# Optimization experiments

Measured on AMD Instinct MI355X. Metric: run time of the kernel, lower is better.

## Reference

```python
import jax, jax.numpy as jnp
import numpy as np

N_HEADS = 16

def setup_inputs() -> dict:
    key = jax.random.key(0)
    ks = jax.random.split(key, 6)
    B, L, D = 1, 2048, 1024
    M = 2048  # max_len
    dh = D // N_HEADS
    s = 0.02
    return {
        "x": jax.random.normal(ks[0], (B, L, D), jnp.float32),
        "Wqkv": jax.random.normal(ks[1], (D, 3 * D), jnp.float32) * s,
        "bqkv": jax.random.normal(ks[2], (3 * D,), jnp.float32) * s,
        "Wout": jax.random.normal(ks[3], (D, D), jnp.float32) * s,
        "bout": jax.random.normal(ks[4], (D,), jnp.float32) * s,
        "rel_emb": jax.random.normal(ks[5], (2 * M - 1, dh), jnp.float32),
    }

def reference(x, Wqkv, bqkv, Wout, bout, rel_emb):
    B, L, D = x.shape
    H = N_HEADS
    dh = D // H
    qkv = x @ Wqkv + bqkv                       # [B,L,3D]
    q, k, v = jnp.split(qkv, 3, axis=-1)
    q = q.reshape(B, L, H, dh).transpose(0, 2, 1, 3)  # [B,H,L,dh]
    k = k.reshape(B, L, H, dh).transpose(0, 2, 1, 3)
    v = v.reshape(B, L, H, dh).transpose(0, 2, 1, 3)
    content = jnp.einsum('bhid,bhjd->bhij', q, k)      # [B,H,L,L]
    rel = jnp.einsum('bhid,rd->bhir', q, rel_emb)      # [B,H,L,2M-1]
    # _skew: F.pad(x,(1,0)); view keeps shape; slice [...,:L]
    rel = jnp.pad(rel, ((0, 0), (0, 0), (0, 0), (1, 0)))[..., :L]
    scores = (content + rel) / jnp.sqrt(jnp.asarray(dh, x.dtype))
    attn = jax.nn.softmax(scores, axis=-1)
    out = jnp.einsum('bhij,bhjd->bhid', attn, v)       # [B,H,L,dh]
    out = out.transpose(0, 2, 1, 3).reshape(B, L, D)
    return out @ Wout + bout
```

## Files before the change

kernel.cpp:

```cpp
#include <hip/hip_runtime.h>
#include <hip/hip_bf16.h>
#include <stdint.h>

typedef __attribute__((ext_vector_type(8))) __bf16 bf16x8;
typedef __attribute__((ext_vector_type(4))) float f32x4;
typedef __attribute__((ext_vector_type(16))) float f32x16;
typedef __attribute__((ext_vector_type(2))) uint32_t u32x2;

#define MFMA16(a, b, c) __builtin_amdgcn_mfma_f32_16x16x32_bf16(a, b, c, 0, 0, 0)
#define MFMA32(a, b, c) __builtin_amdgcn_mfma_f32_32x32x16_bf16(a, b, c, 0, 0, 0)

typedef const __attribute__((address_space(1))) uint32_t* gas_ptr;
typedef __attribute__((address_space(3))) uint32_t* lds_ptr;

static __device__ __forceinline__ ushort f2b(float f) {
  union { float f; uint32_t u; } x; x.f = f;
  uint32_t u = x.u + 0x7fffu + ((x.u >> 16) & 1u);
  return (ushort)(u >> 16);
}

static __device__ __forceinline__ void g2lds16(const void* g, void* l) {
  __builtin_amdgcn_global_load_lds((gas_ptr)(uintptr_t)g, (lds_ptr)(uintptr_t)l, 16, 0, 0);
}

static __device__ __forceinline__ u32x2 plswap(uint32_t a, uint32_t b) {
  return __builtin_amdgcn_permlane32_swap(a, b, false, false);
}
static __device__ __forceinline__ float xhalf_max(float x) {
  u32x2 r = plswap(__float_as_uint(x), __float_as_uint(x));
  return fmaxf(__uint_as_float(r.x), __uint_as_float(r.y));
}
static __device__ __forceinline__ float xhalf_sum(float x) {
  u32x2 r = plswap(__float_as_uint(x), __float_as_uint(x));
  return __uint_as_float(r.x) + __uint_as_float(r.y);
}

__global__ __launch_bounds__(256) void prep(const float* __restrict__ x, ushort* __restrict__ xb,
                                            const float* __restrict__ Wqkv, ushort* __restrict__ w1t,
                                            const float* __restrict__ Wout, ushort* __restrict__ w2t,
                                            int L) {
  const int b = blockIdx.x, t = threadIdx.x;
  const int ncvt = (L * 1024) / (256 * 4);
  if (b < ncvt) {
    int i = (b * 256 + t) * 4;
    float4 v = *(const float4*)(x + i);
    ushort4 o;
    o.x = f2b(v.x); o.y = f2b(v.y); o.z = f2b(v.z); o.w = f2b(v.w);
    *(ushort4*)(xb + i) = o;
    return;
  }
  __shared__ ushort tile[64][65];
  const float* in; ushort* out; int N; int b2;
  const int K = 1024;
  if (b < ncvt + 768) { b2 = b - ncvt; N = 3072; in = Wqkv; out = w1t; }
  else                { b2 = b - ncvt - 768; N = 1024; in = Wout; out = w2t; }
  int nx = b2 % (N >> 6), ky = b2 / (N >> 6);
  int n0 = nx * 64, k0 = ky * 64;
#pragma unroll
  for (int i = 0; i < 16; ++i) {
    int idx = i * 256 + t;
    int r = idx >> 6, c = idx & 63;
    tile[r][c] = f2b(in[(size_t)(k0 + r) * N + n0 + c]);
  }
  __syncthreads();
#pragma unroll
  for (int i = 0; i < 16; ++i) {
    int idx = i * 256 + t;
    int r = idx >> 6, c = idx & 63;
    out[(size_t)(n0 + r) * K + k0 + c] = tile[c][r];
  }
}

template <int BM, int BN, bool BIAS>
__global__ __launch_bounds__(256) void gemm_dbuf(const ushort* __restrict__ A,
                                                 const ushort* __restrict__ Bt,
                                                 float* __restrict__ C,
                                                 const float* __restrict__ bias,
                                                 int M, int N, int K) {
  constexpr int WM = BM / 2, WN = BN / 2, MF = WM / 16, NF = WN / 16;
  constexpr int AI = BM / 32, BI = BN / 32;
  __shared__ ushort lA[2][BM * 64];
  __shared__ ushort lB[2][BN * 64];
  const int t = threadIdx.x, lane = t & 63;
  const int bm = blockIdx.y * BM, bn = blockIdx.x * BN;
  const int wid = t >> 6, wr = wid >> 1, wc = wid & 1;

  f32x4 acc[MF][NF] = {};

  auto STAGE = [&](int bb, int k0) {
#pragma unroll
    for (int i = 0; i < AI; ++i) {
      int ci = i * 256 + t;
      int r = ci >> 3, cs = ci & 7;
      int cg = (cs ^ (r & 7)) * 8;
      g2lds16(A + (size_t)(bm + r) * K + k0 + cg, (ushort*)lA[bb] + ci * 8);
    }
#pragma unroll
    for (int i = 0; i < BI; ++i) {
      int ci = i * 256 + t;
      int r = ci >> 3, cs = ci & 7;
      int cg = (cs ^ (r & 7)) * 8;
      g2lds16(Bt + (size_t)(bn + r) * K + k0 + cg, (ushort*)lB[bb] + ci * 8);
    }
  };

  STAGE(0, 0);
  asm volatile("s_waitcnt vmcnt(0)" ::: "memory");
  __builtin_amdgcn_s_barrier();
  __builtin_amdgcn_sched_barrier(0);

  const int NS = K >> 6;
  int buf = 0;
  for (int s = 0; s < NS; ++s) {
    if (s + 1 < NS) STAGE(buf ^ 1, (s + 1) << 6);
#pragma unroll
    for (int kk = 0; kk < 2; ++kk) {
      bf16x8 af[MF], bfr[NF];
#pragma unroll
      for (int m = 0; m < MF; ++m) {
        int row = wr * WM + m * 16 + (lane & 15);
        int cb = kk * 64 + ((lane >> 4) << 4);
        int sw = cb ^ ((row & 7) << 4);
        af[m] = *(const bf16x8*)((const char*)lA[buf] + row * 128 + sw);
      }
#pragma unroll
      for (int n = 0; n < NF; ++n) {
        int row = wc * WN + n * 16 + (lane & 15);
        int cb = kk * 64 + ((lane >> 4) << 4);
        int sw = cb ^ ((row & 7) << 4);
        bfr[n] = *(const bf16x8*)((const char*)lB[buf] + row * 128 + sw);
      }
#pragma unroll
      for (int m = 0; m < MF; ++m)
#pragma unroll
        for (int n = 0; n < NF; ++n) acc[m][n] = MFMA16(af[m], bfr[n], acc[m][n]);
    }
    asm volatile("s_waitcnt vmcnt(0)" ::: "memory");
    __builtin_amdgcn_s_barrier();
    __builtin_amdgcn_sched_barrier(0);
    buf ^= 1;
  }
#pragma unroll
  for (int m = 0; m < MF; ++m) {
#pragma unroll
    for (int n = 0; n < NF; ++n) {
      int col = bn + wc * WN + n * 16 + (lane & 15);
      float b = BIAS ? bias[col] : 0.f;
#pragma unroll
      for (int r = 0; r < 4; ++r) {
        int row = bm + wr * WM + m * 16 + ((lane >> 4) << 2) + r;
        C[(size_t)row * N + col] = acc[m][n][r] + b;
      }
    }
  }
}

__global__ __launch_bounds__(256) void gemm_qkv(const ushort* __restrict__ A,
                                                const ushort* __restrict__ Bt,
                                                const float* __restrict__ bqkv,
                                                const float* __restrict__ rel,
                                                ushort* __restrict__ Qs,
                                                ushort* __restrict__ Kp,
                                                ushort* __restrict__ Vt, int M) {
  __shared__ ushort lA[2][128 * 64];
  __shared__ ushort lB[2][128 * 64];
  const int K = 1024;
  const int t = threadIdx.x, lane = t & 63;
  const int bm = blockIdx.y * 128, bn = blockIdx.x * 128;
  const int wid = t >> 6, wr = wid >> 1, wc = wid & 1;

  f32x4 acc[4][4] = {};

  auto STAGE = [&](int bb, int k0) {
#pragma unroll
    for (int i = 0; i < 4; ++i) {
      int ci = i * 256 + t;
      int r = ci >> 3, cs = ci & 7;
      int cg = (cs ^ (r & 7)) * 8;
      g2lds16(A + (size_t)(bm + r) * K + k0 + cg, (ushort*)lA[bb] + ci * 8);
      g2lds16(Bt + (size_t)(bn + r) * K + k0 + cg, (ushort*)lB[bb] + ci * 8);
    }
  };

  STAGE(0, 0);
  asm volatile("s_waitcnt vmcnt(0)" ::: "memory");
  __builtin_amdgcn_s_barrier();
  __builtin_amdgcn_sched_barrier(0);

  int buf = 0;
  for (int s = 0; s < 16; ++s) {
    if (s + 1 < 16) STAGE(buf ^ 1, (s + 1) << 6);
#pragma unroll
    for (int kk = 0; kk < 2; ++kk) {
      bf16x8 af[4], bfr[4];
#pragma unroll
      for (int m = 0; m < 4; ++m) {
        int row = wr * 64 + m * 16 + (lane & 15);
        int cb = kk * 64 + ((lane >> 4) << 4);
        int sw = cb ^ ((row & 7) << 4);
        af[m] = *(const bf16x8*)((const char*)lA[buf] + row * 128 + sw);
      }
#pragma unroll
      for (int n = 0; n < 4; ++n) {
        int row = wc * 64 + n * 16 + (lane & 15);
        int cb = kk * 64 + ((lane >> 4) << 4);
        int sw = cb ^ ((row & 7) << 4);
        bfr[n] = *(const bf16x8*)((const char*)lB[buf] + row * 128 + sw);
      }
#pragma unroll
      for (int m = 0; m < 4; ++m)
#pragma unroll
        for (int n = 0; n < 4; ++n) acc[m][n] = MFMA16(af[m], bfr[n], acc[m][n]);
    }
    asm volatile("s_waitcnt vmcnt(0)" ::: "memory");
    __builtin_amdgcn_s_barrier();
    __builtin_amdgcn_sched_barrier(0);
    buf ^= 1;
  }

  const int sec = bn >> 10;
  const int cis_base = bn & 1023;
  if (sec < 2) {
    ushort* dst = (sec == 0) ? Qs : Kp;
    const float scale = (sec == 0) ? 0.18033688f : 1.0f;
#pragma unroll
    for (int m = 0; m < 4; ++m) {
#pragma unroll
      for (int n = 0; n < 4; ++n) {
        int cis = cis_base + wc * 64 + n * 16 + (lane & 15);
        int hh = cis >> 6, dd = cis & 63;
        float b = bqkv[sec * 1024 + cis];
#pragma unroll
        for (int r = 0; r < 4; ++r) {
          int row = bm + wr * 64 + m * 16 + ((lane >> 4) << 2) + r;
          float v = acc[m][n][r] + b;
          if (sec == 1 && row > 0) v += rel[(size_t)(row - 1) * 64 + dd];
          dst[((size_t)hh * M + row) * 64 + dd] = f2b(v * scale);
        }
      }
    }
  } else {
    char* tb = (char*)lA;
#pragma unroll
    for (int m = 0; m < 4; ++m) {
#pragma unroll
      for (int n = 0; n < 4; ++n) {
        int cl = wc * 64 + n * 16 + (lane & 15);
        int ll = wr * 64 + m * 16 + ((lane >> 4) << 2);
        float b = bqkv[2048 + cis_base + cl];
        ushort4 w4;
        w4.x = f2b(acc[m][n][0] + b);
        w4.y = f2b(acc[m][n][1] + b);
        w4.z = f2b(acc[m][n][2] + b);
        w4.w = f2b(acc[m][n][3] + b);
        *(ushort4*)(tb + cl * 256 + ((ll * 2) ^ ((cl & 15) << 4))) = w4;
      }
    }
    __syncthreads();
#pragma unroll
    for (int ps = 0; ps < 8; ++ps) {
      int cl = ps * 16 + (t >> 4);
      int chunk = t & 15;
      uint4 rv = *(const uint4*)(tb + cl * 256 + ((chunk * 16) ^ ((cl & 15) << 4)));
      *(uint4*)(Vt + (size_t)(cis_base + cl) * M + bm + chunk * 8) = rv;
    }
  }
}

__global__ __launch_bounds__(512) void attn6(const ushort* __restrict__ Qs,
                                             const ushort* __restrict__ Kp,
                                             const ushort* __restrict__ Vt,
                                             ushort* __restrict__ O, int L) {
  __shared__ char smem[69632];
  __shared__ float mls[4][2][32];
  const int bid = blockIdx.x;
  const int h = (bid & 7) * 2 + (bid >> 7);
  const int q0 = ((bid >> 3) & 15) * 128;
  const int t = threadIdx.x, lane = t & 63, w = t >> 6;
  const int qt = w & 3, ks = w >> 2;
  const int ql = lane & 31, hi = lane >> 5;
  const int sw = (ql & 7) << 4;
  const ushort* kh = Kp + (size_t)h * L * 64;
  const ushort* vh = Vt + (size_t)h * 64 * L;
  const int half = L >> 1;
  const int NT = half >> 6;

  bf16x8 qf[4];
  {
    const ushort* qrow = Qs + ((size_t)h * L + q0 + qt * 32 + ql) * 64 + hi * 8;
#pragma unroll
    for (int c = 0; c < 4; ++c) qf[c] = *(const bf16x8*)(qrow + c * 16);
  }

  f32x16 ot0 = {}, ot1 = {};
  float m = -1e30f, l = 0.f;

  auto STAGE = [&](int bb, int tt) {
    char* base = smem + bb * 32768;
#pragma unroll
    for (int s = 0; s < 2; ++s) {
      int kb = s * half + tt * 64;
      char* sb = base + s * 16384;
      {
        int key = t >> 3, pch = t & 7;
        g2lds16(kh + (((size_t)(kb + key)) << 6) + ((pch ^ (key & 7)) << 3), sb + t * 16);
      }
      {
        int d = t >> 3, pch = t & 7;
        g2lds16(vh + (size_t)d * L + kb + ((pch ^ (d & 7)) << 3), sb + 8192 + t * 16);
      }
    }
  };

  STAGE(0, 0);
  asm volatile("s_waitcnt vmcnt(0)" ::: "memory");
  __builtin_amdgcn_s_barrier();
  __builtin_amdgcn_sched_barrier(0);

  int buf = 0;
  for (int tt = 0; tt < NT; ++tt) {
    if (tt + 1 < NT) STAGE(buf ^ 1, tt + 1);
    const char* kbuf = smem + buf * 32768 + ks * 16384;
    const char* vbuf = kbuf + 8192;
    f32x16 s0 = {}, s1 = {};
#pragma unroll
    for (int c = 0; c < 4; ++c) {
      bf16x8 k0 = *(const bf16x8*)(kbuf + ql * 128 + (((2 * c + hi) << 4) ^ sw));
      bf16x8 k1 = *(const bf16x8*)(kbuf + (32 + ql) * 128 + (((2 * c + hi) << 4) ^ sw));
      s0 = MFMA32(k0, qf[c], s0);
      s1 = MFMA32(k1, qf[c], s1);
    }
    float mx = fmaxf(s0[0], s1[0]);
#pragma unroll
    for (int i = 1; i < 16; ++i) mx = fmaxf(fmaxf(s0[i], s1[i]), mx);
    mx = xhalf_max(mx);
    if (!__all(mx - m <= 8.0f)) {
      float mn = fmaxf(m, mx);
      float sc = __builtin_amdgcn_exp2f(m - mn);
      m = mn;
      l *= sc;
      ot0 = ot0 * sc;
      ot1 = ot1 * sc;
    }
    float rs = 0.f;
#pragma unroll
    for (int tl = 0; tl < 2; ++tl) {
      f32x16 s = tl ? s1 : s0;
      float p[16];
      float r0 = 0.f, r1 = 0.f;
#pragma unroll
      for (int i = 0; i < 16; i += 2) {
        p[i] = __builtin_amdgcn_exp2f(s[i] - m);
        p[i + 1] = __builtin_amdgcn_exp2f(s[i + 1] - m);
        r0 += p[i];
        r1 += p[i + 1];
      }
      rs += r0 + r1;
      uint32_t a[8];
#pragma unroll
      for (int i = 0; i < 8; ++i) {
        uint32_t r;
        asm("v_cvt_pk_bf16_f32 %0, %1, %2" : "=v"(r) : "v"(p[2 * i]), "v"(p[2 * i + 1]));
        a[i] = r;
      }
      u32x2 s02 = plswap(a[0], a[2]);
      u32x2 s13 = plswap(a[1], a[3]);
      u32x2 s46 = plswap(a[4], a[6]);
      u32x2 s57 = plswap(a[5], a[7]);
      union { uint32_t u[4]; bf16x8 v; } b0, b1;
      b0.u[0] = s02.x; b0.u[1] = s13.x; b0.u[2] = s02.y; b0.u[3] = s13.y;
      b1.u[0] = s46.x; b1.u[1] = s57.x; b1.u[2] = s46.y; b1.u[3] = s57.y;
      bf16x8 v00 = *(const bf16x8*)(vbuf + ql * 128 + (((tl * 4 + hi) << 4) ^ sw));
      bf16x8 v01 = *(const bf16x8*)(vbuf + ql * 128 + (((tl * 4 + 2 + hi) << 4) ^ sw));
      bf16x8 v10 = *(const bf16x8*)(vbuf + (32 + ql) * 128 + (((tl * 4 + hi) << 4) ^ sw));
      bf16x8 v11 = *(const bf16x8*)(vbuf + (32 + ql) * 128 + (((tl * 4 + 2 + hi) << 4) ^ sw));
      ot0 = MFMA32(v00, b0.v, ot0);
      ot0 = MFMA32(v01, b1.v, ot0);
      ot1 = MFMA32(v10, b0.v, ot1);
      ot1 = MFMA32(v11, b1.v, ot1);
    }
    l += xhalf_sum(rs);
    asm volatile("s_waitcnt vmcnt(0)" ::: "memory");
    __builtin_amdgcn_s_barrier();
    __builtin_amdgcn_sched_barrier(0);
    buf ^= 1;
  }

  float* part = (float*)smem;
  float* merged = (float*)(smem + 4 * 64 * 33 * 4);
  if (ks == 1) {
    if (hi == 0) { mls[qt][0][ql] = m; mls[qt][1][ql] = l; }
    float* pq = part + qt * 64 * 33;
#pragma unroll
    for (int r = 0; r < 16; ++r) {
      int d = (r & 3) + 8 * (r >> 2) + 4 * hi;
      pq[d * 33 + ql] = ot0[r];
      pq[(d + 32) * 33 + ql] = ot1[r];
    }
  }
  __syncthreads();
  if (ks == 0) {
    float m1 = mls[qt][0][ql], l1 = mls[qt][1][ql];
    float mg = fmaxf(m, m1);
    float e0 = __builtin_amdgcn_exp2f(m - mg);
    float e1 = __builtin_amdgcn_exp2f(m1 - mg);
    float inv = 1.0f / (l * e0 + l1 * e1);
    float* pq = part + qt * 64 * 33;
    float* mq = merged + qt * 32 * 68;
#pragma unroll
    for (int r = 0; r < 16; ++r) {
      int d = (r & 3) + 8 * (r >> 2) + 4 * hi;
      mq[ql * 68 + d] = (ot0[r] * e0 + pq[d * 33 + ql] * e1) * inv;
      mq[ql * 68 + 32 + d] = (ot1[r] * e0 + pq[(d + 32) * 33 + ql] * e1) * inv;
    }
  }
  __syncthreads();
#pragma unroll
  for (int pss = 0; pss < 2; ++pss) {
    int id = pss * 512 + t;
    int qt2 = id >> 8, row = (id >> 3) & 31, c8 = id & 7;
    const float* mq = merged + qt2 * 32 * 68 + row * 68 + c8 * 8;
    float4 f0 = *(const float4*)mq;
    float4 f1 = *(const float4*)(mq + 4);
    union { ushort us[8]; uint4 u4; } o;
    o.us[0] = f2b(f0.x); o.us[1] = f2b(f0.y); o.us[2] = f2b(f0.z); o.us[3] = f2b(f0.w);
    o.us[4] = f2b(f1.x); o.us[5] = f2b(f1.y); o.us[6] = f2b(f1.z); o.us[7] = f2b(f1.w);
    *(uint4*)(O + (size_t)(q0 + qt2 * 32 + row) * 1024 + h * 64 + c8 * 8) = o.u4;
  }
}

extern "C" void kernel_launch(void* const* d_in, const int* in_sizes, int n_in,
                              void* d_out, int out_size, void* d_ws, size_t ws_size,
                              hipStream_t stream) {
  (void)n_in; (void)out_size; (void)ws_size;
  const float* x    = (const float*)d_in[0];
  const float* Wqkv = (const float*)d_in[1];
  const float* bqkv = (const float*)d_in[2];
  const float* Wout = (const float*)d_in[3];
  const float* bout = (const float*)d_in[4];
  const float* rel  = (const float*)d_in[5];
  float* out = (float*)d_out;
  const int L = in_sizes[0] / 1024;

  char* ws = (char*)d_ws;
  const size_t MB = 1024 * 1024;
  ushort* xb  = (ushort*)(ws);
  ushort* w1t = (ushort*)(ws + 4 * MB);
  ushort* w2t = (ushort*)(ws + 10 * MB);
  ushort* Qsb = (ushort*)(ws + 36 * MB);
  ushort* Kpb = (ushort*)(ws + 40 * MB);
  ushort* Vtb = (ushort*)(ws + 44 * MB);
  ushort* Ob  = (ushort*)(ws + 48 * MB);

  prep<<<dim3((L * 1024) / 1024 + 768 + 256), 256, 0, stream>>>(x, xb, Wqkv, w1t, Wout, w2t, L);
  gemm_qkv<<<dim3(3072 / 128, L / 128), 256, 0, stream>>>(xb, w1t, bqkv, rel, Qsb, Kpb, Vtb, L);
  attn6<<<dim3((L / 128) * 16), 512, 0, stream>>>(Qsb, Kpb, Vtb, Ob, L);
  gemm_dbuf<128, 64, true><<<dim3(1024 / 64, L / 128), 256, 0, stream>>>(Ob, w2t, out, bout, L, 1024, 1024);
}
```

Baseline: 84.99 us.

## Drop attention key-split, use 256-thread blocks and deferred vmcnt waits in GEMMs

Measured after the change: 87.64 us. 1.03x slower.

```diff
diff --git a/kernel.cpp b/kernel.cpp
--- a/kernel.cpp
+++ b/kernel.cpp
@@ -21,6 +21,13 @@
 
 static __device__ __forceinline__ void g2lds16(const void* g, void* l) {
   __builtin_amdgcn_global_load_lds((gas_ptr)(uintptr_t)g, (lds_ptr)(uintptr_t)l, 16, 0, 0);
+}
+
+template <int N> static __device__ __forceinline__ void waitvm() {
+  if constexpr (N == 0) asm volatile("s_waitcnt vmcnt(0)" ::: "memory");
+  else if constexpr (N == 4) asm volatile("s_waitcnt vmcnt(4)" ::: "memory");
+  else if constexpr (N == 6) asm volatile("s_waitcnt vmcnt(6)" ::: "memory");
+  else if constexpr (N == 8) asm volatile("s_waitcnt vmcnt(8)" ::: "memory");
 }
 
 static __device__ __forceinline__ u32x2 plswap(uint32_t a, uint32_t b) {
@@ -105,14 +112,13 @@
   };
 
   STAGE(0, 0);
-  asm volatile("s_waitcnt vmcnt(0)" ::: "memory");
-  __builtin_amdgcn_s_barrier();
-  __builtin_amdgcn_sched_barrier(0);
-
   const int NS = K >> 6;
   int buf = 0;
   for (int s = 0; s < NS; ++s) {
-    if (s + 1 < NS) STAGE(buf ^ 1, (s + 1) << 6);
+    if (s + 1 < NS) { STAGE(buf ^ 1, (s + 1) << 6); waitvm<AI + BI>(); }
+    else            { waitvm<0>(); }
+    __builtin_amdgcn_s_barrier();
+    __builtin_amdgcn_sched_barrier(0);
 #pragma unroll
     for (int kk = 0; kk < 2; ++kk) {
       bf16x8 af[MF], bfr[NF];
@@ -135,7 +141,6 @@
 #pragma unroll
         for (int n = 0; n < NF; ++n) acc[m][n] = MFMA16(af[m], bfr[n], acc[m][n]);
     }
-    asm volatile("s_waitcnt vmcnt(0)" ::: "memory");
     __builtin_amdgcn_s_barrier();
     __builtin_amdgcn_sched_barrier(0);
     buf ^= 1;
@@ -183,13 +188,12 @@
   };
 
   STAGE(0, 0);
-  asm volatile("s_waitcnt vmcnt(0)" ::: "memory");
-  __builtin_amdgcn_s_barrier();
-  __builtin_amdgcn_sched_barrier(0);
-
   int buf = 0;
   for (int s = 0; s < 16; ++s) {
-    if (s + 1 < 16) STAGE(buf ^ 1, (s + 1) << 6);
+    if (s + 1 < 16) { STAGE(buf ^ 1, (s + 1) << 6); waitvm<8>(); }
+    else            { waitvm<0>(); }
+    __builtin_amdgcn_s_barrier();
+    __builtin_amdgcn_sched_barrier(0);
 #pragma unroll
     for (int kk = 0; kk < 2; ++kk) {
       bf16x8 af[4], bfr[4];
@@ -212,7 +216,6 @@
 #pragma unroll
         for (int n = 0; n < 4; ++n) acc[m][n] = MFMA16(af[m], bfr[n], acc[m][n]);
     }
-    asm volatile("s_waitcnt vmcnt(0)" ::: "memory");
     __builtin_amdgcn_s_barrier();
     __builtin_amdgcn_sched_barrier(0);
     buf ^= 1;
@@ -267,23 +270,20 @@
   }
 }
 
-__global__ __launch_bounds__(512) void attn6(const ushort* __restrict__ Qs,
+__global__ __launch_bounds__(256) void attn7(const ushort* __restrict__ Qs,
                                              const ushort* __restrict__ Kp,
                                              const ushort* __restrict__ Vt,
                                              ushort* __restrict__ O, int L) {
-  __shared__ char smem[69632];
-  __shared__ float mls[4][2][32];
+  __shared__ char smem[36864];
   const int bid = blockIdx.x;
-  const int h = (bid & 7) * 2 + (bid >> 7);
-  const int q0 = ((bid >> 3) & 15) * 128;
-  const int t = threadIdx.x, lane = t & 63, w = t >> 6;
-  const int qt = w & 3, ks = w >> 2;
+  const int h = (bid & 7) * 2 + ((bid >> 3) & 1);
+  const int q0 = (bid >> 4) * 128;
+  const int t = threadIdx.x, lane = t & 63, qt = t >> 6;
   const int ql = lane & 31, hi = lane >> 5;
   const int sw = (ql & 7) << 4;
   const ushort* kh = Kp + (size_t)h * L * 64;
   const ushort* vh = Vt + (size_t)h * 64 * L;
-  const int half = L >> 1;
-  const int NT = half >> 6;
+  const int NT = L >> 6;
 
   bf16x8 qf[4];
   {
@@ -296,31 +296,30 @@
   float m = -1e30f, l = 0.f;
 
   auto STAGE = [&](int bb, int tt) {
-    char* base = smem + bb * 32768;
-#pragma unroll
-    for (int s = 0; s < 2; ++s) {
-      int kb = s * half + tt * 64;
-      char* sb = base + s * 16384;
-      {
-        int key = t >> 3, pch = t & 7;
-        g2lds16(kh + (((size_t)(kb + key)) << 6) + ((pch ^ (key & 7)) << 3), sb + t * 16);
-      }
-      {
-        int d = t >> 3, pch = t & 7;
-        g2lds16(vh + (size_t)d * L + kb + ((pch ^ (d & 7)) << 3), sb + 8192 + t * 16);
-      }
+    char* sb = smem + bb * 16384;
+    int kb = tt * 64;
+#pragma unroll
+    for (int p = 0; p < 2; ++p) {
+      int idx = p * 256 + t;
+      int key = idx >> 3, pch = idx & 7;
+      g2lds16(kh + (((size_t)(kb + key)) << 6) + ((pch ^ (key & 7)) << 3), sb + idx * 16);
+    }
+#pragma unroll
+    for (int p = 0; p < 2; ++p) {
+      int idx = p * 256 + t;
+      int d = idx >> 3, pch = idx & 7;
+      g2lds16(vh + (size_t)d * L + kb + ((pch ^ (d & 7)) << 3), sb + 8192 + idx * 16);
     }
   };
 
   STAGE(0, 0);
-  asm volatile("s_waitcnt vmcnt(0)" ::: "memory");
-  __builtin_amdgcn_s_barrier();
-  __builtin_amdgcn_sched_barrier(0);
-
   int buf = 0;
   for (int tt = 0; tt < NT; ++tt) {
-    if (tt + 1 < NT) STAGE(buf ^ 1, tt + 1);
-    const char* kbuf = smem + buf * 32768 + ks * 16384;
+    if (tt + 1 < NT) { STAGE(buf ^ 1, tt + 1); waitvm<4>(); }
+    else             { waitvm<0>(); }
+    __builtin_amdgcn_s_barrier();
+    __builtin_amdgcn_sched_barrier(0);
+    const char* kbuf = smem + buf * 16384;
     const char* vbuf = kbuf + 8192;
     f32x16 s0 = {}, s1 = {};
 #pragma unroll
@@ -380,44 +379,26 @@
       ot1 = MFMA32(v11, b1.v, ot1);
     }
     l += xhalf_sum(rs);
-    asm volatile("s_waitcnt vmcnt(0)" ::: "memory");
     __builtin_amdgcn_s_barrier();
     __builtin_amdgcn_sched_barrier(0);
     buf ^= 1;
   }
 
-  float* part = (float*)smem;
-  float* merged = (float*)(smem + 4 * 64 * 33 * 4);
-  if (ks == 1) {
-    if (hi == 0) { mls[qt][0][ql] = m; mls[qt][1][ql] = l; }
-    float* pq = part + qt * 64 * 33;
+  float* merged = (float*)smem;
+  {
+    float inv = 1.0f / l;
+    float* mq = merged + qt * 32 * 68;
 #pragma unroll
     for (int r = 0; r < 16; ++r) {
       int d = (r & 3) + 8 * (r >> 2) + 4 * hi;
-      pq[d * 33 + ql] = ot0[r];
-      pq[(d + 32) * 33 + ql] = ot1[r];
+      mq[ql * 68 + d] = ot0[r] * inv;
+      mq[ql * 68 + 32 + d] = ot1[r] * inv;
     }
   }
   __syncthreads();
-  if (ks == 0) {
-    float m1 = mls[qt][0][ql], l1 = mls[qt][1][ql];
-    float mg = fmaxf(m, m1);
-    float e0 = __builtin_amdgcn_exp2f(m - mg);
-    float e1 = __builtin_amdgcn_exp2f(m1 - mg);
-    float inv = 1.0f / (l * e0 + l1 * e1);
-    float* pq = part + qt * 64 * 33;
-    float* mq = merged + qt * 32 * 68;
-#pragma unroll
-    for (int r = 0; r < 16; ++r) {
-      int d = (r & 3) + 8 * (r >> 2) + 4 * hi;
-      mq[ql * 68 + d] = (ot0[r] * e0 + pq[d * 33 + ql] * e1) * inv;
-      mq[ql * 68 + 32 + d] = (ot1[r] * e0 + pq[(d + 32) * 33 + ql] * e1) * inv;
-    }
-  }
-  __syncthreads();
-#pragma unroll
-  for (int pss = 0; pss < 2; ++pss) {
-    int id = pss * 512 + t;
+#pragma unroll
+  for (int ps = 0; ps < 4; ++ps) {
+    int id = ps * 256 + t;
     int qt2 = id >> 8, row = (id >> 3) & 31, c8 = id & 7;
     const float* mq = merged + qt2 * 32 * 68 + row * 68 + c8 * 8;
     float4 f0 = *(const float4*)mq;
@@ -454,6 +435,6 @@
 
   prep<<<dim3((L * 1024) / 1024 + 768 + 256), 256, 0, stream>>>(x, xb, Wqkv, w1t, Wout, w2t, L);
   gemm_qkv<<<dim3(3072 / 128, L / 128), 256, 0, stream>>>(xb, w1t, bqkv, rel, Qsb, Kpb, Vtb, L);
-  attn6<<<dim3((L / 128) * 16), 512, 0, stream>>>(Qsb, Kpb, Vtb, Ob, L);
+  attn7<<<dim3((L / 128) * 16), 256, 0, stream>>>(Qsb, Kpb, Vtb, Ob, L);
   gemm_dbuf<128, 64, true><<<dim3(1024 / 64, L / 128), 256, 0, stream>>>(Ob, w2t, out, bout, L, 1024, 1024);
 }
```

## Defer vmcnt waits to keep next-stage prefetch in flight and raise MFMA priority

Applied to the files above, without the earlier changes.

Result: faster. 81.97 us, median of 2 (-3.6%).

```diff
diff --git a/kernel.cpp b/kernel.cpp
--- a/kernel.cpp
+++ b/kernel.cpp
@@ -21,6 +21,13 @@
 
 static __device__ __forceinline__ void g2lds16(const void* g, void* l) {
   __builtin_amdgcn_global_load_lds((gas_ptr)(uintptr_t)g, (lds_ptr)(uintptr_t)l, 16, 0, 0);
+}
+
+template <int N> static __device__ __forceinline__ void waitvm() {
+  if constexpr (N == 0) asm volatile("s_waitcnt vmcnt(0)" ::: "memory");
+  else if constexpr (N == 4) asm volatile("s_waitcnt vmcnt(4)" ::: "memory");
+  else if constexpr (N == 6) asm volatile("s_waitcnt vmcnt(6)" ::: "memory");
+  else if constexpr (N == 8) asm volatile("s_waitcnt vmcnt(8)" ::: "memory");
 }
 
 static __device__ __forceinline__ u32x2 plswap(uint32_t a, uint32_t b) {
@@ -105,14 +112,13 @@
   };
 
   STAGE(0, 0);
-  asm volatile("s_waitcnt vmcnt(0)" ::: "memory");
-  __builtin_amdgcn_s_barrier();
-  __builtin_amdgcn_sched_barrier(0);
-
   const int NS = K >> 6;
   int buf = 0;
   for (int s = 0; s < NS; ++s) {
-    if (s + 1 < NS) STAGE(buf ^ 1, (s + 1) << 6);
+    if (s + 1 < NS) { STAGE(buf ^ 1, (s + 1) << 6); waitvm<AI + BI>(); }
+    else            { waitvm<0>(); }
+    __builtin_amdgcn_s_barrier();
+    __builtin_amdgcn_sched_barrier(0);
 #pragma unroll
     for (int kk = 0; kk < 2; ++kk) {
       bf16x8 af[MF], bfr[NF];
@@ -130,12 +136,13 @@
         int sw = cb ^ ((row & 7) << 4);
         bfr[n] = *(const bf16x8*)((const char*)lB[buf] + row * 128 + sw);
       }
+      __builtin_amdgcn_s_setprio(1);
 #pragma unroll
       for (int m = 0; m < MF; ++m)
 #pragma unroll
         for (int n = 0; n < NF; ++n) acc[m][n] = MFMA16(af[m], bfr[n], acc[m][n]);
-    }
-    asm volatile("s_waitcnt vmcnt(0)" ::: "memory");
+      __builtin_amdgcn_s_setprio(0);
+    }
     __builtin_amdgcn_s_barrier();
     __builtin_amdgcn_sched_barrier(0);
     buf ^= 1;
@@ -183,13 +190,12 @@
   };
 
   STAGE(0, 0);
-  asm volatile("s_waitcnt vmcnt(0)" ::: "memory");
-  __builtin_amdgcn_s_barrier();
-  __builtin_amdgcn_sched_barrier(0);
-
   int buf = 0;
   for (int s = 0; s < 16; ++s) {
-    if (s + 1 < 16) STAGE(buf ^ 1, (s + 1) << 6);
+    if (s + 1 < 16) { STAGE(buf ^ 1, (s + 1) << 6); waitvm<8>(); }
+    else            { waitvm<0>(); }
+    __builtin_amdgcn_s_barrier();
+    __builtin_amdgcn_sched_barrier(0);
 #pragma unroll
     for (int kk = 0; kk < 2; ++kk) {
       bf16x8 af[4], bfr[4];
@@ -207,12 +213,13 @@
         int sw = cb ^ ((row & 7) << 4);
         bfr[n] = *(const bf16x8*)((const char*)lB[buf] + row * 128 + sw);
       }
+      __builtin_amdgcn_s_setprio(1);
 #pragma unroll
       for (int m = 0; m < 4; ++m)
 #pragma unroll
         for (int n = 0; n < 4; ++n) acc[m][n] = MFMA16(af[m], bfr[n], acc[m][n]);
-    }
-    asm volatile("s_waitcnt vmcnt(0)" ::: "memory");
+      __builtin_amdgcn_s_setprio(0);
+    }
     __builtin_amdgcn_s_barrier();
     __builtin_amdgcn_sched_barrier(0);
     buf ^= 1;
@@ -267,7 +274,7 @@
   }
 }
 
-__global__ __launch_bounds__(512) void attn6(const ushort* __restrict__ Qs,
+__global__ __launch_bounds__(512) void attn8(const ushort* __restrict__ Qs,
                                              const ushort* __restrict__ Kp,
                                              const ushort* __restrict__ Vt,
                                              ushort* __restrict__ O, int L) {
@@ -313,16 +320,16 @@
   };
 
   STAGE(0, 0);
-  asm volatile("s_waitcnt vmcnt(0)" ::: "memory");
-  __builtin_amdgcn_s_barrier();
-  __builtin_amdgcn_sched_barrier(0);
-
   int buf = 0;
   for (int tt = 0; tt < NT; ++tt) {
-    if (tt + 1 < NT) STAGE(buf ^ 1, tt + 1);
+    if (tt + 1 < NT) { STAGE(buf ^ 1, tt + 1); waitvm<4>(); }
+    else             { waitvm<0>(); }
+    __builtin_amdgcn_s_barrier();
+    __builtin_amdgcn_sched_barrier(0);
     const char* kbuf = smem + buf * 32768 + ks * 16384;
     const char* vbuf = kbuf + 8192;
     f32x16 s0 = {}, s1 = {};
+    __builtin_amdgcn_s_setprio(1);
 #pragma unroll
     for (int c = 0; c < 4; ++c) {
       bf16x8 k0 = *(const bf16x8*)(kbuf + ql * 128 + (((2 * c + hi) << 4) ^ sw));
@@ -330,6 +337,7 @@
       s0 = MFMA32(k0, qf[c], s0);
       s1 = MFMA32(k1, qf[c], s1);
     }
+    __builtin_amdgcn_s_setprio(0);
     float mx = fmaxf(s0[0], s1[0]);
 #pragma unroll
     for (int i = 1; i < 16; ++i) mx = fmaxf(fmaxf(s0[i], s1[i]), mx);
@@ -374,13 +382,14 @@
       bf16x8 v01 = *(const bf16x8*)(vbuf + ql * 128 + (((tl * 4 + 2 + hi) << 4) ^ sw));
       bf16x8 v10 = *(const bf16x8*)(vbuf + (32 + ql) * 128 + (((tl * 4 + hi) << 4) ^ sw));
       bf16x8 v11 = *(const bf16x8*)(vbuf + (32 + ql) * 128 + (((tl * 4 + 2 + hi) << 4) ^ sw));
+      __builtin_amdgcn_s_setprio(1);
       ot0 = MFMA32(v00, b0.v, ot0);
       ot0 = MFMA32(v01, b1.v, ot0);
       ot1 = MFMA32(v10, b0.v, ot1);
       ot1 = MFMA32(v11, b1.v, ot1);
+      __builtin_amdgcn_s_setprio(0);
     }
     l += xhalf_sum(rs);
-    asm volatile("s_waitcnt vmcnt(0)" ::: "memory");
     __builtin_amdgcn_s_barrier();
     __builtin_amdgcn_sched_barrier(0);
     buf ^= 1;
@@ -454,6 +463,6 @@
 
   prep<<<dim3((L * 1024) / 1024 + 768 + 256), 256, 0, stream>>>(x, xb, Wqkv, w1t, Wout, w2t, L);
   gemm_qkv<<<dim3(3072 / 128, L / 128), 256, 0, stream>>>(xb, w1t, bqkv, rel, Qsb, Kpb, Vtb, L);
-  attn6<<<dim3((L / 128) * 16), 512, 0, stream>>>(Qsb, Kpb, Vtb, Ob, L);
+  attn8<<<dim3((L / 128) * 16), 512, 0, stream>>>(Qsb, Kpb, Vtb, Ob, L);
   gemm_dbuf<128, 64, true><<<dim3(1024 / 64, L / 128), 256, 0, stream>>>(Ob, w2t, out, bout, L, 1024, 1024);
 }
```
